# Kernel tuning notes

Measured on AMD Instinct MI355X. Metric: run time of the kernel, lower is better.

Reference implementation:

```python
import jax, jax.numpy as jnp
import numpy as np

N, L, S, D, H, DK = 4, 2048, 2048, 1024, 16, 64


def setup_inputs() -> dict:
    key = jax.random.key(0)
    kq, kk, kv, kwq, kwo = jax.random.split(key, 5)
    Q = jax.random.normal(kq, (N, L, D), dtype=jnp.float32)
    K = jax.random.normal(kk, (N, S, D), dtype=jnp.float32)
    V = jax.random.normal(kv, (N, S, D), dtype=jnp.float32)
    # per-head query projection weights (the source reuses Lq for K and V too)
    Wq = jax.random.normal(kwq, (H, DK, D), dtype=jnp.float32) * (D ** -0.5)
    # output projection Lo: Linear(h*dv -> Dv), weight shape (out, in)
    Wo = jax.random.normal(kwo, (D, H * DK), dtype=jnp.float32) * ((H * DK) ** -0.5)
    return {"Q": Q, "K": K, "V": V, "Wq": Wq, "Wo": Wo}


def reference(Q, K, V, Wq, Wo):
    dk = Wq.shape[1]
    # Faithful to source: ALL of q, k, v are projected with the Lq weights.
    q = jnp.einsum('nld,hkd->hnlk', Q, Wq)   # (H,N,L,dk)
    k = jnp.einsum('nsd,hkd->hnsk', K, Wq)   # (H,N,S,dk)
    v = jnp.einsum('nsd,hkd->hnsk', V, Wq)   # (H,N,S,dk)
    scale = jnp.asarray(dk, Q.dtype) ** 0.5
    scores = jnp.einsum('hnlk,hnsk->hnls', q, k) / scale  # (H,N,L,S)
    # Faithful to F.softmax(dot) with no dim on a 3D tensor: torch picks dim=0
    # (the batch axis N); here that is axis=1 of the head-stacked (H,N,L,S).
    attn = jax.nn.softmax(scores, axis=1)
    heads = jnp.einsum('hnls,hnsk->hnlk', attn, v)        # (H,N,L,dk)
    # concat heads along last dim -> (N,L,H*dk)
    heads = jnp.transpose(heads, (1, 2, 0, 3)).reshape(Q.shape[0], Q.shape[1], -1)
    return heads @ Wo.T  # (N,L,Dv)
```

## Files before the change

kernel.cpp:

```cpp
#include <hip/hip_runtime.h>
#include <hip/hip_bf16.h>

typedef __attribute__((ext_vector_type(8))) short short8;
typedef __attribute__((ext_vector_type(4))) short short4v;
typedef __attribute__((ext_vector_type(4))) float float4v;

#define DEVI static __device__ __forceinline__

#if __has_builtin(__builtin_amdgcn_exp2f)
#define EXP2(x) __builtin_amdgcn_exp2f(x)
#else
#define EXP2(x) exp2f(x)
#endif

DEVI unsigned short f2bf(float f) {
  unsigned int u = __builtin_bit_cast(unsigned int, f);
  u += 0x7fffu + ((u >> 16) & 1u);
  return (unsigned short)(u >> 16);
}

DEVI void gload16(const void* src, void* lds_dst) {
  __builtin_amdgcn_global_load_lds(
      (const __attribute__((address_space(1))) void*)src,
      (__attribute__((address_space(3))) void*)lds_dst, 16, 0, 0);
}

template<int AF32, int CMODE>
__global__ __launch_bounds__(256, 2)
void gemm_bt128(const void* __restrict__ Ap, const float* __restrict__ Bp,
                void* __restrict__ Cp, int M, int Nc, int Kd, float oscale)
{
  __shared__ alignas(16) short As[128 * 40];
  __shared__ alignas(16) short Bs[128 * 40];

  const int tid = threadIdx.x;
  const int lane = tid & 63;
  const int wid = tid >> 6;
  const int rl = lane & 15;
  const int g = lane >> 4;
  const int bm = blockIdx.x * 128;
  const int bn = blockIdx.y * 128;
  const int wm = (wid >> 1) * 64;
  const int wn = (wid & 1) * 64;
  const int srow = tid >> 1;
  const int k0 = (tid & 1) * 16;

  float4v acc[4][4];
#pragma unroll
  for (int i = 0; i < 4; ++i)
#pragma unroll
    for (int j = 0; j < 4; ++j) acc[i][j] = (float4v)(0.0f);

  const float* Af = (const float*)Ap;
  const unsigned short* Ab = (const unsigned short*)Ap;

  float4v afr[4], bfr[4];
  short8 ah[2], bh[2];

  const int NK = Kd >> 5;

  auto loadA = [&](int ks) {
    size_t base = (size_t)(bm + srow) * Kd + ks * 32 + k0;
    if constexpr (AF32 != 0) {
      afr[0] = *(const float4v*)(Af + base);
      afr[1] = *(const float4v*)(Af + base + 4);
      afr[2] = *(const float4v*)(Af + base + 8);
      afr[3] = *(const float4v*)(Af + base + 12);
    } else {
      ah[0] = *(const short8*)(Ab + base);
      ah[1] = *(const short8*)(Ab + base + 8);
    }
  };
  auto loadB = [&](int ks) {
    size_t base = (size_t)(bn + srow) * Kd + ks * 32 + k0;
    bfr[0] = *(const float4v*)(Bp + base);
    bfr[1] = *(const float4v*)(Bp + base + 4);
    bfr[2] = *(const float4v*)(Bp + base + 8);
    bfr[3] = *(const float4v*)(Bp + base + 12);
  };

  loadA(0);
  loadB(0);

  for (int ks = 0; ks < NK; ++ks) {
    if constexpr (AF32 != 0) {
      short8 r0, r1;
#pragma unroll
      for (int j = 0; j < 4; ++j) {
        r0[j]     = (short)f2bf(afr[0][j]);
        r0[4 + j] = (short)f2bf(afr[1][j]);
        r1[j]     = (short)f2bf(afr[2][j]);
        r1[4 + j] = (short)f2bf(afr[3][j]);
      }
      ah[0] = r0; ah[1] = r1;
    }
    {
      short8 r0, r1;
#pragma unroll
      for (int j = 0; j < 4; ++j) {
        r0[j]     = (short)f2bf(bfr[0][j]);
        r0[4 + j] = (short)f2bf(bfr[1][j]);
        r1[j]     = (short)f2bf(bfr[2][j]);
        r1[4 + j] = (short)f2bf(bfr[3][j]);
      }
      bh[0] = r0; bh[1] = r1;
    }
    __syncthreads();
    *(short8*)(As + srow * 40 + k0)     = ah[0];
    *(short8*)(As + srow * 40 + k0 + 8) = ah[1];
    *(short8*)(Bs + srow * 40 + k0)     = bh[0];
    *(short8*)(Bs + srow * 40 + k0 + 8) = bh[1];
    __syncthreads();
    if (ks + 1 < NK) { loadA(ks + 1); loadB(ks + 1); }

    short8 a8[4], b8[4];
#pragma unroll
    for (int mt = 0; mt < 4; ++mt)
      a8[mt] = *(const short8*)(As + (wm + mt * 16 + rl) * 40 + 8 * g);
#pragma unroll
    for (int nt = 0; nt < 4; ++nt)
      b8[nt] = *(const short8*)(Bs + (wn + nt * 16 + rl) * 40 + 8 * g);
#pragma unroll
    for (int mt = 0; mt < 4; ++mt)
#pragma unroll
      for (int nt = 0; nt < 4; ++nt)
        acc[mt][nt] = __builtin_amdgcn_mfma_f32_16x16x32_bf16(a8[mt], b8[nt], acc[mt][nt], 0, 0, 0);
  }

#pragma unroll
  for (int mt = 0; mt < 4; ++mt)
#pragma unroll
    for (int nt = 0; nt < 4; ++nt) {
      const int col = bn + wn + nt * 16 + rl;
      const int row0 = bm + wm + mt * 16 + 4 * g;
      if constexpr (CMODE == 1) {
        float* C = (float*)Cp;
#pragma unroll
        for (int r = 0; r < 4; ++r)
          C[(size_t)(row0 + r) * Nc + col] = acc[mt][nt][r];
      } else if constexpr (CMODE == 0) {
        unsigned short* C = (unsigned short*)Cp;
#pragma unroll
        for (int r = 0; r < 4; ++r)
          C[(size_t)(row0 + r) * Nc + col] = f2bf(acc[mt][nt][r] * oscale);
      } else {
        unsigned short* C = (unsigned short*)Cp;
        unsigned w0 = (unsigned)f2bf(acc[mt][nt][0]) | ((unsigned)f2bf(acc[mt][nt][1]) << 16);
        unsigned w1 = (unsigned)f2bf(acc[mt][nt][2]) | ((unsigned)f2bf(acc[mt][nt][3]) << 16);
        uint2 val; val.x = w0; val.y = w1;
        *(uint2*)(C + (size_t)col * M + row0) = val;
      }
    }
}

__global__ __launch_bounds__(512, 2)
void attn_bn(const unsigned short* __restrict__ qb,
             const unsigned short* __restrict__ kb,
             const unsigned short* __restrict__ vtb,
             unsigned short* __restrict__ hb)
{
  __shared__ alignas(128) char smem[131072];

  const int tid = threadIdx.x;
  const int lane = tid & 63;
  const int wid = tid >> 6;
  const int rl = lane & 15;
  const int g = lane >> 4;
  const int h = blockIdx.y;
  const int l0 = blockIdx.x * 128 + wid * 16;

  short8 qf[4][2];
#pragma unroll
  for (int n = 0; n < 4; ++n)
#pragma unroll
    for (int dh = 0; dh < 2; ++dh)
      qf[n][dh] = *(const short8*)(qb + (size_t)(n * 2048 + l0 + rl) * 1024 + h * 64 + dh * 32 + 8 * g);

  float4v ha[4][4];
#pragma unroll
  for (int n = 0; n < 4; ++n)
#pragma unroll
    for (int t = 0; t < 4; ++t) ha[n][t] = (float4v)(0.0f);

  const size_t koff0 = ((size_t)(wid * 2048) + (size_t)(lane >> 3)) * 1024
                     + (size_t)(h * 64) + (size_t)(((lane & 7) ^ (lane >> 3)) * 8);
  const size_t voff0 = ((size_t)(h * 64) + (size_t)(lane >> 2)) * 8192
                     + (size_t)((wid - 4) * 2048)
                     + (size_t)((((lane & 3) ^ ((lane >> 3) & 3)) * 8));

  auto stage = [&](int step, int b) {
    if (wid < 4) {
      char* kdst = smem + b * 32768 + wid * 4096;
      const unsigned short* ksrc = kb + koff0 + (size_t)step * 32 * 1024;
#pragma unroll
      for (int ii = 0; ii < 4; ++ii)
        gload16(ksrc + ii * 8192, kdst + ii * 1024);
    } else {
      char* vdst = smem + b * 32768 + 16384 + (wid - 4) * 4096;
      const unsigned short* vsrc = vtb + voff0 + (size_t)step * 32;
#pragma unroll
      for (int ii = 0; ii < 4; ++ii)
        gload16(vsrc + (size_t)ii * 16 * 8192, vdst + ii * 1024);
    }
  };

  stage(0, 0);
  stage(1, 1);
  stage(2, 2);
  asm volatile("s_waitcnt vmcnt(8)" ::: "memory");
  __builtin_amdgcn_s_barrier();

  const unsigned xr = ((unsigned)((rl >> 1) & 3)) << 4;
  const unsigned half = ((unsigned)(g & 1)) << 3;

  for (int to = 0; to < 16; ++to) {
#pragma unroll
    for (int ti = 0; ti < 4; ++ti) {
      const int t = to * 4 + ti;
      char* kbase = smem + ti * 32768;
      char* vbase = kbase + 16384;

      float4v sc[4][2];
#pragma unroll
      for (int n = 0; n < 4; ++n) {
        char* kn = kbase + n * 4096;
#pragma unroll
        for (int ss = 0; ss < 2; ++ss) {
          const int srw = ss * 16 + rl;
          const unsigned sw = ((unsigned)(srw & 7)) << 4;
          short8 kf0 = *(const short8*)(kn + srw * 128 + ((16u * (unsigned)g) ^ sw));
          short8 kf1 = *(const short8*)(kn + srw * 128 + ((64u + 16u * (unsigned)g) ^ sw));
          float4v c = (float4v)(0.0f);
          c = __builtin_amdgcn_mfma_f32_16x16x32_bf16(kf0, qf[n][0], c, 0, 0, 0);
          c = __builtin_amdgcn_mfma_f32_16x16x32_bf16(kf1, qf[n][1], c, 0, 0, 0);
          sc[n][ss] = c;
        }
      }

#pragma unroll
      for (int ss = 0; ss < 2; ++ss) {
        float ex[4][4];
#pragma unroll
        for (int n = 0; n < 4; ++n)
#pragma unroll
          for (int r = 0; r < 4; ++r) {
            float e = EXP2(sc[n][ss][r]);
            ex[n][r] = fminf(fmaxf(e, 1e-30f), 1.7e7f);
          }
#pragma unroll
        for (int r = 0; r < 4; ++r) {
          float inv = __builtin_amdgcn_rcpf(ex[0][r] + ex[1][r] + ex[2][r] + ex[3][r]);
          ex[0][r] *= inv; ex[1][r] *= inv; ex[2][r] *= inv; ex[3][r] *= inv;
        }
        short4v pf[4];
#pragma unroll
        for (int n = 0; n < 4; ++n) {
          unsigned lo = (unsigned)f2bf(ex[n][0]) | ((unsigned)f2bf(ex[n][1]) << 16);
          unsigned hi = (unsigned)f2bf(ex[n][2]) | ((unsigned)f2bf(ex[n][3]) << 16);
          uint2 u; u.x = lo; u.y = hi;
          pf[n] = __builtin_bit_cast(short4v, u);
        }

        const unsigned chunk0 = 2u * (unsigned)ss + ((unsigned)g >> 1);
#pragma unroll
        for (int n = 0; n < 4; ++n) {
          char* vn = vbase + n * 4096;
#pragma unroll
          for (int t4 = 0; t4 < 4; ++t4) {
            const char* rowp = vn + (t4 * 16 + rl) * 64;
            short4v va = *(const short4v*)(rowp + (((chunk0 << 4) ^ xr) + half));
            ha[n][t4] = __builtin_amdgcn_mfma_f32_16x16x16bf16_1k(va, pf[n], ha[n][t4], 0, 0, 0);
          }
        }
      }

      if (t + 3 < 64) stage(t + 3, (ti + 3) & 3);
      asm volatile("s_waitcnt vmcnt(8)" ::: "memory");
      __builtin_amdgcn_s_barrier();
    }
  }

#pragma unroll
  for (int n = 0; n < 4; ++n)
#pragma unroll
    for (int tt = 0; tt < 4; ++tt) {
      unsigned w0 = (unsigned)f2bf(ha[n][tt][0]) | ((unsigned)f2bf(ha[n][tt][1]) << 16);
      unsigned w1 = (unsigned)f2bf(ha[n][tt][2]) | ((unsigned)f2bf(ha[n][tt][3]) << 16);
      size_t off = (size_t)(n * 2048 + l0 + rl) * 1024 + h * 64 + tt * 16 + 4 * g;
      uint2 val; val.x = w0; val.y = w1;
      *(uint2*)(hb + off) = val;
    }
}

extern "C" void kernel_launch(void* const* d_in, const int* in_sizes, int n_in,
                              void* d_out, int out_size, void* d_ws, size_t ws_size,
                              hipStream_t stream)
{
  const float* Q  = (const float*)d_in[0];
  const float* K  = (const float*)d_in[1];
  const float* V  = (const float*)d_in[2];
  const float* Wq = (const float*)d_in[3];
  const float* Wo = (const float*)d_in[4];
  float* out = (float*)d_out;

  unsigned short* qb = (unsigned short*)d_ws;
  unsigned short* kw = qb + (size_t)8192 * 1024;
  unsigned short* vt = kw + (size_t)8192 * 1024;
  unsigned short* hw = qb;

  const float CS = 0.18033688011112042f;

  dim3 gg(64, 8), bb(256);
  gemm_bt128<1, 0><<<gg, bb, 0, stream>>>(Q, Wq, qb, 8192, 1024, 1024, CS);
  gemm_bt128<1, 0><<<gg, bb, 0, stream>>>(K, Wq, kw, 8192, 1024, 1024, 1.0f);
  gemm_bt128<1, 2><<<gg, bb, 0, stream>>>(V, Wq, vt, 8192, 1024, 1024, 1.0f);
  attn_bn<<<dim3(16, 16), dim3(512), 0, stream>>>(qb, kw, vt, hw);
  gemm_bt128<0, 1><<<gg, bb, 0, stream>>>(hw, Wo, out, 8192, 1024, 1024, 1.0f);
}
```

Baseline: 277.5 us.

## Merge PV MFMAs into 16x16x32 and use hardware bf16 packing

```diff
diff --git a/kernel.cpp b/kernel.cpp
--- a/kernel.cpp
+++ b/kernel.cpp
@@ -17,6 +17,26 @@
   unsigned int u = __builtin_bit_cast(unsigned int, f);
   u += 0x7fffu + ((u >> 16) & 1u);
   return (unsigned short)(u >> 16);
+}
+
+DEVI short8 pack8(float4v a, float4v b) {
+  struct P4 { __hip_bfloat162 x, y, z, w; } t;
+  t.x = __float22bfloat162_rn(make_float2(a[0], a[1]));
+  t.y = __float22bfloat162_rn(make_float2(a[2], a[3]));
+  t.z = __float22bfloat162_rn(make_float2(b[0], b[1]));
+  t.w = __float22bfloat162_rn(make_float2(b[2], b[3]));
+  short8 r;
+  __builtin_memcpy(&r, &t, 16);
+  return r;
+}
+
+DEVI short4v pack4(float a, float b, float c, float d) {
+  struct P2 { __hip_bfloat162 x, y; } t;
+  t.x = __float22bfloat162_rn(make_float2(a, b));
+  t.y = __float22bfloat162_rn(make_float2(c, d));
+  short4v r;
+  __builtin_memcpy(&r, &t, 8);
+  return r;
 }
 
 DEVI void gload16(const void* src, void* lds_dst) {
@@ -84,27 +104,11 @@
 
   for (int ks = 0; ks < NK; ++ks) {
     if constexpr (AF32 != 0) {
-      short8 r0, r1;
-#pragma unroll
-      for (int j = 0; j < 4; ++j) {
-        r0[j]     = (short)f2bf(afr[0][j]);
-        r0[4 + j] = (short)f2bf(afr[1][j]);
-        r1[j]     = (short)f2bf(afr[2][j]);
-        r1[4 + j] = (short)f2bf(afr[3][j]);
-      }
-      ah[0] = r0; ah[1] = r1;
-    }
-    {
-      short8 r0, r1;
-#pragma unroll
-      for (int j = 0; j < 4; ++j) {
-        r0[j]     = (short)f2bf(bfr[0][j]);
-        r0[4 + j] = (short)f2bf(bfr[1][j]);
-        r1[j]     = (short)f2bf(bfr[2][j]);
-        r1[4 + j] = (short)f2bf(bfr[3][j]);
-      }
-      bh[0] = r0; bh[1] = r1;
-    }
+      ah[0] = pack8(afr[0], afr[1]);
+      ah[1] = pack8(afr[2], afr[3]);
+    }
+    bh[0] = pack8(bfr[0], bfr[1]);
+    bh[1] = pack8(bfr[2], bfr[3]);
     __syncthreads();
     *(short8*)(As + srow * 40 + k0)     = ah[0];
     *(short8*)(As + srow * 40 + k0 + 8) = ah[1];
@@ -145,10 +149,8 @@
           C[(size_t)(row0 + r) * Nc + col] = f2bf(acc[mt][nt][r] * oscale);
       } else {
         unsigned short* C = (unsigned short*)Cp;
-        unsigned w0 = (unsigned)f2bf(acc[mt][nt][0]) | ((unsigned)f2bf(acc[mt][nt][1]) << 16);
-        unsigned w1 = (unsigned)f2bf(acc[mt][nt][2]) | ((unsigned)f2bf(acc[mt][nt][3]) << 16);
-        uint2 val; val.x = w0; val.y = w1;
-        *(uint2*)(C + (size_t)col * M + row0) = val;
+        short4v w = pack4(acc[mt][nt][0], acc[mt][nt][1], acc[mt][nt][2], acc[mt][nt][3]);
+        *(short4v*)(C + (size_t)col * M + row0) = w;
       }
     }
 }
@@ -212,6 +214,8 @@
 
   const unsigned xr = ((unsigned)((rl >> 1) & 3)) << 4;
   const unsigned half = ((unsigned)(g & 1)) << 3;
+  const unsigned voff_lo = (((((unsigned)g >> 1) << 4) ^ xr) + half);
+  const unsigned voff_hi = ((((2u + ((unsigned)g >> 1)) << 4) ^ xr) + half);
 
   for (int to = 0; to < 16; ++to) {
 #pragma unroll
@@ -237,40 +241,36 @@
         }
       }
 
+      short4v pf[2][4];
 #pragma unroll
       for (int ss = 0; ss < 2; ++ss) {
         float ex[4][4];
 #pragma unroll
         for (int n = 0; n < 4; ++n)
 #pragma unroll
-          for (int r = 0; r < 4; ++r) {
-            float e = EXP2(sc[n][ss][r]);
-            ex[n][r] = fminf(fmaxf(e, 1e-30f), 1.7e7f);
-          }
+          for (int r = 0; r < 4; ++r)
+            ex[n][r] = EXP2(fminf(sc[n][ss][r], 24.0f));
 #pragma unroll
         for (int r = 0; r < 4; ++r) {
-          float inv = __builtin_amdgcn_rcpf(ex[0][r] + ex[1][r] + ex[2][r] + ex[3][r]);
+          float inv = __builtin_amdgcn_rcpf((ex[0][r] + ex[1][r]) + (ex[2][r] + ex[3][r]) + 1e-30f);
           ex[0][r] *= inv; ex[1][r] *= inv; ex[2][r] *= inv; ex[3][r] *= inv;
         }
-        short4v pf[4];
-#pragma unroll
-        for (int n = 0; n < 4; ++n) {
-          unsigned lo = (unsigned)f2bf(ex[n][0]) | ((unsigned)f2bf(ex[n][1]) << 16);
-          unsigned hi = (unsigned)f2bf(ex[n][2]) | ((unsigned)f2bf(ex[n][3]) << 16);
-          uint2 u; u.x = lo; u.y = hi;
-          pf[n] = __builtin_bit_cast(short4v, u);
-        }
-
-        const unsigned chunk0 = 2u * (unsigned)ss + ((unsigned)g >> 1);
-#pragma unroll
-        for (int n = 0; n < 4; ++n) {
-          char* vn = vbase + n * 4096;
-#pragma unroll
-          for (int t4 = 0; t4 < 4; ++t4) {
-            const char* rowp = vn + (t4 * 16 + rl) * 64;
-            short4v va = *(const short4v*)(rowp + (((chunk0 << 4) ^ xr) + half));
-            ha[n][t4] = __builtin_amdgcn_mfma_f32_16x16x16bf16_1k(va, pf[n], ha[n][t4], 0, 0, 0);
-          }
+#pragma unroll
+        for (int n = 0; n < 4; ++n)
+          pf[ss][n] = pack4(ex[n][0], ex[n][1], ex[n][2], ex[n][3]);
+      }
+
+#pragma unroll
+      for (int n = 0; n < 4; ++n) {
+        char* vn = vbase + n * 4096;
+        short8 pf8 = __builtin_shufflevector(pf[0][n], pf[1][n], 0, 1, 2, 3, 4, 5, 6, 7);
+#pragma unroll
+        for (int t4 = 0; t4 < 4; ++t4) {
+          const char* rowp = vn + (t4 * 16 + rl) * 64;
+          short4v lo = *(const short4v*)(rowp + voff_lo);
+          short4v hi = *(const short4v*)(rowp + voff_hi);
+          short8 va8 = __builtin_shufflevector(lo, hi, 0, 1, 2, 3, 4, 5, 6, 7);
+          ha[n][t4] = __builtin_amdgcn_mfma_f32_16x16x32_bf16(va8, pf8, ha[n][t4], 0, 0, 0);
         }
       }
 
@@ -284,11 +284,9 @@
   for (int n = 0; n < 4; ++n)
 #pragma unroll
     for (int tt = 0; tt < 4; ++tt) {
-      unsigned w0 = (unsigned)f2bf(ha[n][tt][0]) | ((unsigned)f2bf(ha[n][tt][1]) << 16);
-      unsigned w1 = (unsigned)f2bf(ha[n][tt][2]) | ((unsigned)f2bf(ha[n][tt][3]) << 16);
+      short4v w = pack4(ha[n][tt][0], ha[n][tt][1], ha[n][tt][2], ha[n][tt][3]);
       size_t off = (size_t)(n * 2048 + l0 + rl) * 1024 + h * 64 + tt * 16 + 4 * g;
-      uint2 val; val.x = w0; val.y = w1;
-      *(uint2*)(hb + off) = val;
+      *(short4v*)(hb + off) = w;
     }
 }
 
```

New measurement: 274.8 us. Within noise of the previous version (-1.0%).
